# Kernel tuning notes

Hardware: AMD Instinct MI355X
Metric: run time of the kernel (lower is better)

## Reference

```python
import jax, jax.numpy as jnp
import numpy as np

ALPHA = 0.2  # LeakyReLU negative slope
MASK_VAL = -9e15


def setup_inputs() -> dict:
    key = jax.random.key(0)
    k1, k2, k3 = jax.random.split(key, 3)
    bs, N, d = 16, 1024, 128
    h = jax.random.normal(k1, (bs, N, d), dtype=jnp.float32)
    # nn.Linear(in, out, bias=False).weight has shape [out, in]
    W = jax.random.normal(k2, (d, d), dtype=jnp.float32) * (1.414 / np.sqrt(d))
    # a: Linear(2*out, 1) -> weight [1, 2d] flattened to [2d], bias [1]
    a_w = jax.random.normal(k3, (2 * d,), dtype=jnp.float32) * 0.1
    a_b = jnp.zeros((1,), dtype=jnp.float32)
    return {"h": h, "W": W, "a_w": a_w, "a_b": a_b}


def reference(h, W, a_w, a_b):
    # h: [bs, N, d], W: [d, d] (torch Linear weight), a_w: [2d], a_b: [1]
    bs, N, d = h.shape
    Wh = jnp.einsum('bnd,fd->bnf', h, W)  # [bs, N, d]
    # Decompose a([Wh_i ; Wh_j]) = Wh_i . a1 + Wh_j . a2 + b  (avoids O(N^2 * 2d) concat)
    a1, a2 = a_w[:d], a_w[d:]
    s1 = Wh @ a1  # [bs, N] -- source-node contribution (row index i)
    s2 = Wh @ a2  # [bs, N] -- target-node contribution (col index j)
    e = jax.nn.leaky_relu(s1[:, :, None] + s2[:, None, :] + a_b[0], negative_slope=ALPHA)
    # adj = ones - eye: mask out the diagonal (self-edges)
    diag = jnp.eye(N, dtype=bool)
    e = jnp.where(diag[None, :, :], MASK_VAL, e)
    attention = jax.nn.softmax(e, axis=-1)  # [bs, N, N]
    h_prime = jnp.einsum('bij,bjf->bif', attention, Wh)
    return jax.nn.elu(h_prime)  # concat=True applies ELU
```

## Files before the change

kernel.cpp:

```cpp
#include <hip/hip_runtime.h>
#include <hip/hip_bf16.h>
#include <stdint.h>

#define LOG2E 1.4426950408889634f

typedef float f32x4 __attribute__((ext_vector_type(4)));
typedef short s16x8 __attribute__((ext_vector_type(8)));
typedef int   i32x4 __attribute__((ext_vector_type(4)));

__device__ __forceinline__ float bf2f(uint16_t u) {
    uint32_t x = ((uint32_t)u) << 16;
    float f;
    __builtin_memcpy(&f, &x, 4);
    return f;
}
__device__ __forceinline__ uint16_t f2bf(float f) {
    uint32_t x;
    __builtin_memcpy(&x, &f, 4);
    uint32_t r = (x + 0x7fffu + ((x >> 16) & 1u)) >> 16;
    return (uint16_t)r;
}

__global__ __launch_bounds__(256) void k0_splitW(
    const float* __restrict__ W, uint16_t* __restrict__ whi, uint16_t* __restrict__ wlo)
{
    int i = blockIdx.x * 256 + threadIdx.x;
    float x = W[i];
    uint16_t hb = f2bf(x);
    whi[i] = hb;
    wlo[i] = f2bf(x - bf2f(hb));
}

__global__ __launch_bounds__(256) void k1_gemm(
    const float* __restrict__ h, const uint16_t* __restrict__ whi_,
    const uint16_t* __restrict__ wlo_,
    const float* __restrict__ aw, const float* __restrict__ ab,
    uint16_t* __restrict__ whB, float* __restrict__ s1b,
    float* __restrict__ E1g, float* __restrict__ E2g,
    float* __restrict__ smaxrg)
{
    __shared__ float sred[4][16][2];
    const int tid = threadIdx.x;
    const int w = tid >> 6, lane = tid & 63;
    const int q = lane >> 4, n16 = lane & 15;
    const int R0 = blockIdx.x * 16;
    const int f0 = w * 32;

    f32x4 acc[2];
    acc[0] = 0.f; acc[1] = 0.f;

    const float* hrow = h + (size_t)(R0 + n16) * 128 + q * 8;
    const uint16_t* whbase = whi_ + (size_t)(f0 + n16) * 128 + q * 8;
    const uint16_t* wlbase = wlo_ + (size_t)(f0 + n16) * 128 + q * 8;
#pragma unroll
    for (int kc = 0; kc < 4; ++kc) {
        float4 x0 = *(const float4*)(hrow + kc * 32);
        float4 x1 = *(const float4*)(hrow + kc * 32 + 4);
        float xs[8] = {x0.x, x0.y, x0.z, x0.w, x1.x, x1.y, x1.z, x1.w};
        s16x8 ahi, alo;
#pragma unroll
        for (int t = 0; t < 8; ++t) {
            uint16_t hb = f2bf(xs[t]);
            ahi[t] = (short)hb;
            alo[t] = (short)f2bf(xs[t] - bf2f(hb));
        }
#pragma unroll
        for (int fb = 0; fb < 2; ++fb) {
            s16x8 bhi = *(const s16x8*)(whbase + fb * 16 * 128 + kc * 32);
            s16x8 blo = *(const s16x8*)(wlbase + fb * 16 * 128 + kc * 32);
            acc[fb] = __builtin_amdgcn_mfma_f32_16x16x32_bf16(ahi, bhi, acc[fb], 0, 0, 0);
            acc[fb] = __builtin_amdgcn_mfma_f32_16x16x32_bf16(alo, bhi, acc[fb], 0, 0, 0);
            acc[fb] = __builtin_amdgcn_mfma_f32_16x16x32_bf16(ahi, blo, acc[fb], 0, 0, 0);
        }
    }

    float s1p[4] = {0.f, 0.f, 0.f, 0.f}, s2p[4] = {0.f, 0.f, 0.f, 0.f};
#pragma unroll
    for (int fb = 0; fb < 2; ++fb) {
        float a1 = aw[f0 + fb * 16 + n16];
        float a2 = aw[128 + f0 + fb * 16 + n16];
#pragma unroll
        for (int reg = 0; reg < 4; ++reg) {
            s1p[reg] = fmaf(acc[fb][reg], a1, s1p[reg]);
            s2p[reg] = fmaf(acc[fb][reg], a2, s2p[reg]);
        }
    }
#pragma unroll
    for (int off = 1; off < 16; off <<= 1) {
#pragma unroll
        for (int reg = 0; reg < 4; ++reg) {
            s1p[reg] += __shfl_xor(s1p[reg], off);
            s2p[reg] += __shfl_xor(s2p[reg], off);
        }
    }
    if (n16 == 0) {
#pragma unroll
        for (int reg = 0; reg < 4; ++reg) {
            sred[w][q * 4 + reg][0] = s1p[reg];
            sred[w][q * 4 + reg][1] = s2p[reg];
        }
    }
    __syncthreads();
    if (tid < 16) {
        float s1 = sred[0][tid][0] + sred[1][tid][0] + sred[2][tid][0] + sred[3][tid][0];
        float s2 = sred[0][tid][1] + sred[1][tid][1] + sred[2][tid][1] + sred[3][tid][1];
        int R = R0 + tid;
        s1b[R] = LOG2E * (s1 + ab[0]);
        float s2s = LOG2E * s2;
        E1g[R] = __builtin_amdgcn_exp2f(s2s);
        E2g[R] = __builtin_amdgcn_exp2f(0.2f * s2s);
        float m = s2s;
#pragma unroll
        for (int off = 1; off < 16; off <<= 1)
            m = fmaxf(m, __shfl_xor(m, off));
        if (tid == 0) smaxrg[blockIdx.x] = m;
    }

    const int b = R0 >> 10;
    const int jt = (R0 & 1023) >> 5;
    const int rg1 = (R0 >> 4) & 1;
    uint16_t* base = whB + (size_t)b * 131072 + (size_t)jt * 512;
    const int lane8p = (rg1 * 2 + (q >> 1)) * 16 + n16;
#pragma unroll
    for (int fb = 0; fb < 2; ++fb) {
        int fblk = w * 2 + fb;
        uint32_t e0 = f2bf(acc[fb][0]), e1 = f2bf(acc[fb][1]);
        uint32_t e2 = f2bf(acc[fb][2]), e3 = f2bf(acc[fb][3]);
        uint2 val = make_uint2(e0 | (e1 << 16), e2 | (e3 << 16));
        *(uint2*)(base + fblk * 16384 + lane8p * 8 + (q & 1) * 4) = val;
    }
}

__global__ __launch_bounds__(128, 4) void k2_attn(
    const uint16_t* __restrict__ whB, const float* __restrict__ s1b,
    const float* __restrict__ E1g, const float* __restrict__ E2g,
    const float* __restrict__ smaxrg, float* __restrict__ out)
{
    __shared__ float red[2][12][64];
    const int tid = threadIdx.x;
    const int wv = tid >> 6;
    const int lane = tid & 63;
    const int q = lane >> 4, n16 = lane & 15;
    const int idx = blockIdx.x;
    const int xcd = idx & 7;
    const int o = idx >> 3;
    const int b = ((o >> 7) << 3) | xcd;
    const int rem = o & 127;
    const int rg = rem >> 2;
    const int fq = rem & 3;
    const int jb = b << 10;
    const int iw0 = rg * 32;
    const int f0 = fq * 32;

    float M = smaxrg[(b << 6) | lane];
#pragma unroll
    for (int off = 1; off < 64; off <<= 1)
        M = fmaxf(M, __shfl_xor(M, off));

    float eA[2], eB[2];
#pragma unroll
    for (int rf = 0; rf < 2; ++rf) {
        float s1v = s1b[jb + iw0 + rf * 16 + n16];
        float tm = s1v + M;
        float mi = fmaxf(tm, 0.2f * tm);
        eA[rf] = __builtin_amdgcn_exp2f(s1v - mi);
        eB[rf] = __builtin_amdgcn_exp2f(fmaf(0.2f, s1v, -mi));
    }

    f32x4 acc[2][2], accl[2];
#pragma unroll
    for (int rf = 0; rf < 2; ++rf) {
        acc[rf][0] = 0.f; acc[rf][1] = 0.f; accl[rf] = 0.f;
    }

    s16x8 Bones;
#pragma unroll
    for (int t = 0; t < 8; ++t) Bones[t] = (short)0x3F80;

    const int fblk0 = fq * 2, fblk1 = fq * 2 + 1;
    const int jt0 = wv << 4;
    const uint16_t* wb = whB + ((size_t)b << 17) + lane * 8;
    const uint16_t* wb0 = wb + jt0 * 512;
    const float* e1q = E1g + jb + jt0 * 32 + q * 8;
    const float* e2q = E2g + jb + jt0 * 32 + q * 8;

    s16x8 Bc0 = *(const s16x8*)(wb0 + fblk0 * 16384);
    s16x8 Bc1 = *(const s16x8*)(wb0 + fblk1 * 16384);
    float4 c1a = *(const float4*)(e1q);
    float4 c1b = *(const float4*)(e1q + 4);
    float4 c2a = *(const float4*)(e2q);
    float4 c2b = *(const float4*)(e2q + 4);

    for (int t = 0; t < 16; ++t) {
        const int tn = (t < 15) ? t + 1 : 15;
        const uint16_t* bpn = wb0 + tn * 512;
        s16x8 Bn0 = *(const s16x8*)(bpn + fblk0 * 16384);
        s16x8 Bn1 = *(const s16x8*)(bpn + fblk1 * 16384);
        float4 n1a = *(const float4*)(e1q + tn * 32);
        float4 n1b = *(const float4*)(e1q + tn * 32 + 4);
        float4 n2a = *(const float4*)(e2q + tn * 32);
        float4 n2b = *(const float4*)(e2q + tn * 32 + 4);

        float e1v[8] = {c1a.x, c1a.y, c1a.z, c1a.w, c1b.x, c1b.y, c1b.z, c1b.w};
        float e2v[8] = {c2a.x, c2a.y, c2a.z, c2a.w, c2b.x, c2b.y, c2b.z, c2b.w};

        s16x8 A[2];
#pragma unroll
        for (int rf = 0; rf < 2; ++rf) {
            i32x4 pk;
#pragma unroll
            for (int pr = 0; pr < 4; ++pr) {
                float p0 = fmaxf(eA[rf] * e1v[2 * pr],     eB[rf] * e2v[2 * pr]);
                float p1 = fmaxf(eA[rf] * e1v[2 * pr + 1], eB[rf] * e2v[2 * pr + 1]);
                pk[pr] = (int)__builtin_amdgcn_perm(
                    __builtin_bit_cast(uint32_t, p1),
                    __builtin_bit_cast(uint32_t, p0), 0x07060302u);
            }
            A[rf] = __builtin_bit_cast(s16x8, pk);
        }
#pragma unroll
        for (int rf = 0; rf < 2; ++rf) {
            acc[rf][0] = __builtin_amdgcn_mfma_f32_16x16x32_bf16(A[rf], Bc0, acc[rf][0], 0, 0, 0);
            acc[rf][1] = __builtin_amdgcn_mfma_f32_16x16x32_bf16(A[rf], Bc1, acc[rf][1], 0, 0, 0);
            accl[rf]   = __builtin_amdgcn_mfma_f32_16x16x32_bf16(A[rf], Bones, accl[rf], 0, 0, 0);
        }
        Bc0 = Bn0; Bc1 = Bn1;
        c1a = n1a; c1b = n1b; c2a = n2a; c2b = n2b;
    }

    const int orf = 1 - wv;
#pragma unroll
    for (int fb = 0; fb < 2; ++fb)
#pragma unroll
        for (int reg = 0; reg < 4; ++reg)
            red[wv][fb * 4 + reg][lane] = acc[orf][fb][reg];
#pragma unroll
    for (int reg = 0; reg < 4; ++reg)
        red[wv][8 + reg][lane] = accl[orf][reg];
    __syncthreads();
#pragma unroll
    for (int fb = 0; fb < 2; ++fb)
#pragma unroll
        for (int reg = 0; reg < 4; ++reg)
            acc[wv][fb][reg] += red[orf][fb * 4 + reg][lane];
#pragma unroll
    for (int reg = 0; reg < 4; ++reg)
        accl[wv][reg] += red[orf][8 + reg][lane];

    {
        const int rf = wv;
#pragma unroll
        for (int reg = 0; reg < 4; ++reg) {
            int iw = iw0 + rf * 16 + q * 4 + reg;
            float s1v = s1b[jb + iw];
            float tm = s1v + M;
            float mi = fmaxf(tm, 0.2f * tm);
            float eAr = __builtin_amdgcn_exp2f(s1v - mi);
            float eBr = __builtin_amdgcn_exp2f(fmaf(0.2f, s1v, -mi));
            float p = fmaxf(eAr * E1g[jb + iw], eBr * E2g[jb + iw]);
            float pt = __builtin_bit_cast(float, __builtin_bit_cast(uint32_t, p) & 0xffff0000u);
            accl[rf][reg] -= pt;
            int lane_i = ((iw >> 3) & 3) * 16 + n16;
#pragma unroll
            for (int fb = 0; fb < 2; ++fb) {
                size_t a = ((size_t)b << 17) + (size_t)(fq * 2 + fb) * 16384 +
                           (size_t)(iw >> 5) * 512 + lane_i * 8 + (iw & 7);
                float wv_ = bf2f(whB[a]);
                acc[rf][fb][reg] -= pt * wv_;
            }
        }
    }

    {
        const int rf = wv;
#pragma unroll
        for (int reg = 0; reg < 4; ++reg) {
            float rl = 1.0f / accl[rf][reg];
            int row = jb + iw0 + rf * 16 + q * 4 + reg;
#pragma unroll
            for (int fb = 0; fb < 2; ++fb) {
                float v = acc[rf][fb][reg] * rl;
                float e = v > 0.f ? v : (__builtin_amdgcn_exp2f(v * LOG2E) - 1.f);
                out[(size_t)row * 128 + f0 + fb * 16 + n16] = e;
            }
        }
    }
}

extern "C" void kernel_launch(void* const* d_in, const int* in_sizes, int n_in,
                              void* d_out, int out_size, void* d_ws, size_t ws_size,
                              hipStream_t stream) {
    (void)in_sizes; (void)n_in; (void)out_size; (void)ws_size;
    const float* h  = (const float*)d_in[0];
    const float* W  = (const float*)d_in[1];
    const float* aw = (const float*)d_in[2];
    const float* ab = (const float*)d_in[3];
    float* out = (float*)d_out;

    uint16_t* whB = (uint16_t*)d_ws;
    float* s1b    = (float*)((char*)d_ws + (4u << 20));
    float* E1g    = s1b + 16384;
    float* E2g    = E1g + 16384;
    float* smaxrg = E2g + 16384;
    uint16_t* whi = (uint16_t*)(smaxrg + 1024);
    uint16_t* wlo = whi + 16384;

    k0_splitW<<<64, 256, 0, stream>>>(W, whi, wlo);
    k1_gemm<<<1024, 256, 0, stream>>>(h, whi, wlo, aw, ab, whB, s1b, E1g, E2g, smaxrg);
    k2_attn<<<2048, 128, 0, stream>>>(whB, s1b, E1g, E2g, smaxrg, out);
}
```

Measured before the change: 107.4 us.

## Restructure attention kernel work split and dedupe h bf16 split via LDS

In the attention kernel, the old split had two waves each covering half the j range for 32 rows, followed by a cross-wave LDS reduction. Each wave now covers all 1024 j for its own 16 rows and 64 features (4 MFMA column blocks), which removes the shared-memory reduction and its barrier. The grid goes from 2048 blocks of 128 threads to 512 blocks of 256. The GEMM kernel now converts h into hi/lo bf16 once per block into LDS rather than redundantly in each wave. Paired multiplies use f32x2 vectors so the compiler can emit packed math. The trade-off is a longer serial loop per wave and fewer blocks, with more B-fragment registers live at once.

```diff
diff --git a/kernel.cpp b/kernel.cpp
--- a/kernel.cpp
+++ b/kernel.cpp
@@ -5,6 +5,7 @@
 #define LOG2E 1.4426950408889634f
 
 typedef float f32x4 __attribute__((ext_vector_type(4)));
+typedef float f32x2 __attribute__((ext_vector_type(2)));
 typedef short s16x8 __attribute__((ext_vector_type(8)));
 typedef int   i32x4 __attribute__((ext_vector_type(4)));
 
@@ -39,6 +40,8 @@
     float* __restrict__ E1g, float* __restrict__ E2g,
     float* __restrict__ smaxrg)
 {
+    __shared__ uint16_t ahi_s[256 * 8];
+    __shared__ uint16_t alo_s[256 * 8];
     __shared__ float sred[4][16][2];
     const int tid = threadIdx.x;
     const int w = tid >> 6, lane = tid & 63;
@@ -46,24 +49,35 @@
     const int R0 = blockIdx.x * 16;
     const int f0 = w * 32;
 
+    {
+        const int r  = tid & 15;
+        const int qq = (tid >> 4) & 3;
+        const int kc = tid >> 6;
+        const float* hp = h + (size_t)(R0 + r) * 128 + kc * 32 + qq * 8;
+        float4 x0 = *(const float4*)(hp);
+        float4 x1 = *(const float4*)(hp + 4);
+        float xs[8] = {x0.x, x0.y, x0.z, x0.w, x1.x, x1.y, x1.z, x1.w};
+        s16x8 hi8, lo8;
+#pragma unroll
+        for (int t = 0; t < 8; ++t) {
+            uint16_t hb = f2bf(xs[t]);
+            hi8[t] = (short)hb;
+            lo8[t] = (short)f2bf(xs[t] - bf2f(hb));
+        }
+        *(s16x8*)(ahi_s + tid * 8) = hi8;
+        *(s16x8*)(alo_s + tid * 8) = lo8;
+    }
+    __syncthreads();
+
     f32x4 acc[2];
     acc[0] = 0.f; acc[1] = 0.f;
 
-    const float* hrow = h + (size_t)(R0 + n16) * 128 + q * 8;
     const uint16_t* whbase = whi_ + (size_t)(f0 + n16) * 128 + q * 8;
     const uint16_t* wlbase = wlo_ + (size_t)(f0 + n16) * 128 + q * 8;
 #pragma unroll
     for (int kc = 0; kc < 4; ++kc) {
-        float4 x0 = *(const float4*)(hrow + kc * 32);
-        float4 x1 = *(const float4*)(hrow + kc * 32 + 4);
-        float xs[8] = {x0.x, x0.y, x0.z, x0.w, x1.x, x1.y, x1.z, x1.w};
-        s16x8 ahi, alo;
-#pragma unroll
-        for (int t = 0; t < 8; ++t) {
-            uint16_t hb = f2bf(xs[t]);
-            ahi[t] = (short)hb;
-            alo[t] = (short)f2bf(xs[t] - bf2f(hb));
-        }
+        s16x8 ahi = *(const s16x8*)(ahi_s + (kc * 64 + lane) * 8);
+        s16x8 alo = *(const s16x8*)(alo_s + (kc * 64 + lane) * 8);
 #pragma unroll
         for (int fb = 0; fb < 2; ++fb) {
             s16x8 bhi = *(const s16x8*)(whbase + fb * 16 * 128 + kc * 32);
@@ -131,12 +145,11 @@
     }
 }
 
-__global__ __launch_bounds__(128, 4) void k2_attn(
+__global__ __launch_bounds__(256, 2) void k2_attn(
     const uint16_t* __restrict__ whB, const float* __restrict__ s1b,
     const float* __restrict__ E1g, const float* __restrict__ E2g,
     const float* __restrict__ smaxrg, float* __restrict__ out)
 {
-    __shared__ float red[2][12][64];
     const int tid = threadIdx.x;
     const int wv = tid >> 6;
     const int lane = tid & 63;
@@ -144,58 +157,58 @@
     const int idx = blockIdx.x;
     const int xcd = idx & 7;
     const int o = idx >> 3;
-    const int b = ((o >> 7) << 3) | xcd;
-    const int rem = o & 127;
-    const int rg = rem >> 2;
-    const int fq = rem & 3;
+    const int b = ((o >> 5) << 3) | xcd;
+    const int rem = o & 31;
+    const int rg = rem >> 1;
+    const int fh = rem & 1;
     const int jb = b << 10;
-    const int iw0 = rg * 32;
-    const int f0 = fq * 32;
+    const int iw0 = rg * 64 + wv * 16;
+    const int f0 = fh * 64;
 
     float M = smaxrg[(b << 6) | lane];
 #pragma unroll
     for (int off = 1; off < 64; off <<= 1)
         M = fmaxf(M, __shfl_xor(M, off));
 
-    float eA[2], eB[2];
-#pragma unroll
-    for (int rf = 0; rf < 2; ++rf) {
-        float s1v = s1b[jb + iw0 + rf * 16 + n16];
+    f32x2 eA2, eB2;
+    {
+        float s1v = s1b[jb + iw0 + n16];
         float tm = s1v + M;
         float mi = fmaxf(tm, 0.2f * tm);
-        eA[rf] = __builtin_amdgcn_exp2f(s1v - mi);
-        eB[rf] = __builtin_amdgcn_exp2f(fmaf(0.2f, s1v, -mi));
-    }
-
-    f32x4 acc[2][2], accl[2];
-#pragma unroll
-    for (int rf = 0; rf < 2; ++rf) {
-        acc[rf][0] = 0.f; acc[rf][1] = 0.f; accl[rf] = 0.f;
-    }
+        float ea = __builtin_amdgcn_exp2f(s1v - mi);
+        float eb = __builtin_amdgcn_exp2f(fmaf(0.2f, s1v, -mi));
+        eA2[0] = ea; eA2[1] = ea;
+        eB2[0] = eb; eB2[1] = eb;
+    }
+
+    f32x4 acc[4], accl;
+#pragma unroll
+    for (int fb = 0; fb < 4; ++fb) acc[fb] = 0.f;
+    accl = 0.f;
 
     s16x8 Bones;
 #pragma unroll
     for (int t = 0; t < 8; ++t) Bones[t] = (short)0x3F80;
 
-    const int fblk0 = fq * 2, fblk1 = fq * 2 + 1;
-    const int jt0 = wv << 4;
-    const uint16_t* wb = whB + ((size_t)b << 17) + lane * 8;
-    const uint16_t* wb0 = wb + jt0 * 512;
-    const float* e1q = E1g + jb + jt0 * 32 + q * 8;
-    const float* e2q = E2g + jb + jt0 * 32 + q * 8;
-
-    s16x8 Bc0 = *(const s16x8*)(wb0 + fblk0 * 16384);
-    s16x8 Bc1 = *(const s16x8*)(wb0 + fblk1 * 16384);
+    const uint16_t* wbt = whB + ((size_t)b << 17) + (size_t)fh * 65536 + lane * 8;
+    const float* e1q = E1g + jb + q * 8;
+    const float* e2q = E2g + jb + q * 8;
+
+    s16x8 Bc[4];
+#pragma unroll
+    for (int fb = 0; fb < 4; ++fb)
+        Bc[fb] = *(const s16x8*)(wbt + fb * 16384);
     float4 c1a = *(const float4*)(e1q);
     float4 c1b = *(const float4*)(e1q + 4);
     float4 c2a = *(const float4*)(e2q);
     float4 c2b = *(const float4*)(e2q + 4);
 
-    for (int t = 0; t < 16; ++t) {
-        const int tn = (t < 15) ? t + 1 : 15;
-        const uint16_t* bpn = wb0 + tn * 512;
-        s16x8 Bn0 = *(const s16x8*)(bpn + fblk0 * 16384);
-        s16x8 Bn1 = *(const s16x8*)(bpn + fblk1 * 16384);
+    for (int t = 0; t < 32; ++t) {
+        const int tn = (t < 31) ? t + 1 : 31;
+        s16x8 Bn[4];
+#pragma unroll
+        for (int fb = 0; fb < 4; ++fb)
+            Bn[fb] = *(const s16x8*)(wbt + fb * 16384 + tn * 512);
         float4 n1a = *(const float4*)(e1q + tn * 32);
         float4 n1b = *(const float4*)(e1q + tn * 32 + 4);
         float4 n2a = *(const float4*)(e2q + tn * 32);
@@ -204,85 +217,63 @@
         float e1v[8] = {c1a.x, c1a.y, c1a.z, c1a.w, c1b.x, c1b.y, c1b.z, c1b.w};
         float e2v[8] = {c2a.x, c2a.y, c2a.z, c2a.w, c2b.x, c2b.y, c2b.z, c2b.w};
 
-        s16x8 A[2];
-#pragma unroll
-        for (int rf = 0; rf < 2; ++rf) {
+        s16x8 A;
+        {
             i32x4 pk;
 #pragma unroll
             for (int pr = 0; pr < 4; ++pr) {
-                float p0 = fmaxf(eA[rf] * e1v[2 * pr],     eB[rf] * e2v[2 * pr]);
-                float p1 = fmaxf(eA[rf] * e1v[2 * pr + 1], eB[rf] * e2v[2 * pr + 1]);
+                f32x2 e1p; e1p[0] = e1v[2 * pr]; e1p[1] = e1v[2 * pr + 1];
+                f32x2 e2p; e2p[0] = e2v[2 * pr]; e2p[1] = e2v[2 * pr + 1];
+                f32x2 m1 = eA2 * e1p;
+                f32x2 m2 = eB2 * e2p;
+                float p0 = fmaxf(m1[0], m2[0]);
+                float p1 = fmaxf(m1[1], m2[1]);
                 pk[pr] = (int)__builtin_amdgcn_perm(
                     __builtin_bit_cast(uint32_t, p1),
                     __builtin_bit_cast(uint32_t, p0), 0x07060302u);
             }
-            A[rf] = __builtin_bit_cast(s16x8, pk);
-        }
-#pragma unroll
-        for (int rf = 0; rf < 2; ++rf) {
-            acc[rf][0] = __builtin_amdgcn_mfma_f32_16x16x32_bf16(A[rf], Bc0, acc[rf][0], 0, 0, 0);
-            acc[rf][1] = __builtin_amdgcn_mfma_f32_16x16x32_bf16(A[rf], Bc1, acc[rf][1], 0, 0, 0);
-            accl[rf]   = __builtin_amdgcn_mfma_f32_16x16x32_bf16(A[rf], Bones, accl[rf], 0, 0, 0);
-        }
-        Bc0 = Bn0; Bc1 = Bn1;
+            A = __builtin_bit_cast(s16x8, pk);
+        }
+#pragma unroll
+        for (int fb = 0; fb < 4; ++fb)
+            acc[fb] = __builtin_amdgcn_mfma_f32_16x16x32_bf16(A, Bc[fb], acc[fb], 0, 0, 0);
+        accl = __builtin_amdgcn_mfma_f32_16x16x32_bf16(A, Bones, accl, 0, 0, 0);
+
+#pragma unroll
+        for (int fb = 0; fb < 4; ++fb) Bc[fb] = Bn[fb];
         c1a = n1a; c1b = n1b; c2a = n2a; c2b = n2b;
     }
 
-    const int orf = 1 - wv;
-#pragma unroll
-    for (int fb = 0; fb < 2; ++fb)
-#pragma unroll
-        for (int reg = 0; reg < 4; ++reg)
-            red[wv][fb * 4 + reg][lane] = acc[orf][fb][reg];
-#pragma unroll
-    for (int reg = 0; reg < 4; ++reg)
-        red[wv][8 + reg][lane] = accl[orf][reg];
-    __syncthreads();
-#pragma unroll
-    for (int fb = 0; fb < 2; ++fb)
-#pragma unroll
-        for (int reg = 0; reg < 4; ++reg)
-            acc[wv][fb][reg] += red[orf][fb * 4 + reg][lane];
-#pragma unroll
-    for (int reg = 0; reg < 4; ++reg)
-        accl[wv][reg] += red[orf][8 + reg][lane];
-
-    {
-        const int rf = wv;
-#pragma unroll
-        for (int reg = 0; reg < 4; ++reg) {
-            int iw = iw0 + rf * 16 + q * 4 + reg;
-            float s1v = s1b[jb + iw];
-            float tm = s1v + M;
-            float mi = fmaxf(tm, 0.2f * tm);
-            float eAr = __builtin_amdgcn_exp2f(s1v - mi);
-            float eBr = __builtin_amdgcn_exp2f(fmaf(0.2f, s1v, -mi));
-            float p = fmaxf(eAr * E1g[jb + iw], eBr * E2g[jb + iw]);
-            float pt = __builtin_bit_cast(float, __builtin_bit_cast(uint32_t, p) & 0xffff0000u);
-            accl[rf][reg] -= pt;
-            int lane_i = ((iw >> 3) & 3) * 16 + n16;
-#pragma unroll
-            for (int fb = 0; fb < 2; ++fb) {
-                size_t a = ((size_t)b << 17) + (size_t)(fq * 2 + fb) * 16384 +
-                           (size_t)(iw >> 5) * 512 + lane_i * 8 + (iw & 7);
-                float wv_ = bf2f(whB[a]);
-                acc[rf][fb][reg] -= pt * wv_;
-            }
-        }
-    }
-
-    {
-        const int rf = wv;
-#pragma unroll
-        for (int reg = 0; reg < 4; ++reg) {
-            float rl = 1.0f / accl[rf][reg];
-            int row = jb + iw0 + rf * 16 + q * 4 + reg;
-#pragma unroll
-            for (int fb = 0; fb < 2; ++fb) {
-                float v = acc[rf][fb][reg] * rl;
-                float e = v > 0.f ? v : (__builtin_amdgcn_exp2f(v * LOG2E) - 1.f);
-                out[(size_t)row * 128 + f0 + fb * 16 + n16] = e;
-            }
+#pragma unroll
+    for (int reg = 0; reg < 4; ++reg) {
+        int iw = iw0 + q * 4 + reg;
+        float s1v = s1b[jb + iw];
+        float tm = s1v + M;
+        float mi = fmaxf(tm, 0.2f * tm);
+        float eAr = __builtin_amdgcn_exp2f(s1v - mi);
+        float eBr = __builtin_amdgcn_exp2f(fmaf(0.2f, s1v, -mi));
+        float p = fmaxf(eAr * E1g[jb + iw], eBr * E2g[jb + iw]);
+        float pt = __builtin_bit_cast(float, __builtin_bit_cast(uint32_t, p) & 0xffff0000u);
+        accl[reg] -= pt;
+        int lane_i = ((iw >> 3) & 3) * 16 + n16;
+#pragma unroll
+        for (int fb = 0; fb < 4; ++fb) {
+            size_t a = ((size_t)b << 17) + (size_t)(fh * 4 + fb) * 16384 +
+                       (size_t)(iw >> 5) * 512 + lane_i * 8 + (iw & 7);
+            float wv_ = bf2f(whB[a]);
+            acc[fb][reg] -= pt * wv_;
+        }
+    }
+
+#pragma unroll
+    for (int reg = 0; reg < 4; ++reg) {
+        float rl = 1.0f / accl[reg];
+        int row = jb + iw0 + q * 4 + reg;
+#pragma unroll
+        for (int fb = 0; fb < 4; ++fb) {
+            float v = acc[fb][reg] * rl;
+            float e = v > 0.f ? v : (__builtin_amdgcn_exp2f(v * LOG2E) - 1.f);
+            out[(size_t)row * 128 + f0 + fb * 16 + n16] = e;
         }
     }
 }
@@ -307,5 +298,5 @@
 
     k0_splitW<<<64, 256, 0, stream>>>(W, whi, wlo);
     k1_gemm<<<1024, 256, 0, stream>>>(h, whi, wlo, aw, ab, whB, s1b, E1g, E2g, smaxrg);
-    k2_attn<<<2048, 128, 0, stream>>>(whB, s1b, E1g, E2g, smaxrg, out);
-}
+    k2_attn<<<512, 256, 0, stream>>>(whB, s1b, E1g, E2g, smaxrg, out);
+}
```

Measured after the change: 93.16 us (median of 2 runs). 13.3% less time.
